# Performance work log

Hardware: AMD Instinct MI355X
Metric: run time of the kernel (lower is better)

## Reference

```python
import jax, jax.numpy as jnp
import numpy as np
from jax import lax

B, C, H, W = 16, 3, 512, 512


def _nms(heat):
    # 3x3 max-pool, stride 1, SAME padding; keep only local peaks
    hmax = lax.reduce_window(heat, -jnp.inf, lax.max,
                             (1, 1, 3, 3), (1, 1, 1, 1), 'SAME')
    return heat * (hmax == heat).astype(heat.dtype)


def _topk(scores, K):
    b, c, h, w = scores.shape
    # per-class topk over the spatial plane
    topk_scores, topk_inds = lax.top_k(scores.reshape(b, c, h * w), K)  # [b,c,K]
    topk_row = (topk_inds // w).astype(scores.dtype)
    topk_col = (topk_inds % w).astype(scores.dtype)
    # global topk across (class, K)
    topk_score, topk_ind = lax.top_k(topk_scores.reshape(b, c * K), K)  # [b,K]
    topk_clses = topk_ind // K
    gath = lambda x: jnp.take_along_axis(x.reshape(b, c * K), topk_ind, axis=1)
    return topk_score, gath(topk_inds), topk_clses, gath(topk_row), gath(topk_col)


def _transpose_and_gather_feat(feat, inds):
    b, ch, h, w = feat.shape
    f = feat.transpose(0, 2, 3, 1).reshape(b, h * w, ch)  # [b,HW,ch]
    return jnp.take_along_axis(f, inds[:, :, None], axis=1)  # [b,K,ch]


def _decode(hm, cen_offset, direction, z_coor, dim, K):
    b = hm.shape[0]
    hm = _nms(hm)
    scores, inds, clses, row, col = _topk(hm, K)
    off = _transpose_and_gather_feat(cen_offset, inds)           # [b,K,2]
    col = col[:, :, None] + off[:, :, 0:1]
    row = row[:, :, None] + off[:, :, 1:2]
    direction = _transpose_and_gather_feat(direction, inds)      # [b,K,2]
    z_coor = _transpose_and_gather_feat(z_coor, inds)            # [b,K,1]
    dim = _transpose_and_gather_feat(dim, inds)                  # [b,K,3]
    clses = clses[:, :, None].astype(hm.dtype)
    scores = scores[:, :, None]
    return jnp.concatenate([scores, col, row, z_coor, dim, direction, clses], axis=2)


def setup_inputs() -> dict:
    key = jax.random.key(0)
    k1, k2, k3, k4, k5 = jax.random.split(key, 5)
    return {
        'hm_cen': jax.random.normal(k1, (B, C, H, W), jnp.float32),
        'cen_offset': jax.random.normal(k2, (B, 2, H, W), jnp.float32),
        'direction': jax.random.normal(k3, (B, 2, H, W), jnp.float32),
        'z_coor': jax.random.normal(k4, (B, 1, H, W), jnp.float32),
        'dim': jax.random.normal(k5, (B, 3, H, W), jnp.float32),
        'K': 500,
    }


def reference(hm_cen, cen_offset, direction, z_coor, dim, K):
    # postprocessing_v2 applies sigmoid to the class heatmap before decode
    heat = jax.nn.sigmoid(hm_cen)
    return _decode(heat, cen_offset, direction, z_coor, dim, K)  # [B,K,10]
```

## Files before the change

kernel.cpp:

```cpp
#include <hip/hip_runtime.h>
#include <math.h>
#include <float.h>

#define Hd 512
#define Wd 512
#define HWp (Hd*Wd)
#define Bn 16
#define Cn 3
#define NMAP (Bn*Cn)
#define KTOP 500
#define P_SPLIT 8
#define BAND 64
#define SCAP 4096

__device__ __forceinline__ uint32_t flipbits(float v){
  uint32_t u = __float_as_uint(v);
  return u ^ (0x80000000u | (uint32_t)(-(int32_t)(u>>31)));
}
__device__ __forceinline__ float unflipbits(uint32_t f){
  uint32_t u = f ^ ((f>>31)? 0x80000000u : 0xFFFFFFFFu);
  return __uint_as_float(u);
}

__device__ __forceinline__ void nms_row(
    const float4 p0, const float4 p1, const float4 c0, const float4 c1,
    const float4 n0, const float4 n1, const int lane,
    uint32_t& pk, float* cv)
{
  float vm0 = fmaxf(fmaxf(p0.x,c0.x),n0.x);
  float vm1 = fmaxf(fmaxf(p0.y,c0.y),n0.y);
  float vm2 = fmaxf(fmaxf(p0.z,c0.z),n0.z);
  float vm3 = fmaxf(fmaxf(p0.w,c0.w),n0.w);
  float vm4 = fmaxf(fmaxf(p1.x,c1.x),n1.x);
  float vm5 = fmaxf(fmaxf(p1.y,c1.y),n1.y);
  float vm6 = fmaxf(fmaxf(p1.z,c1.z),n1.z);
  float vm7 = fmaxf(fmaxf(p1.w,c1.w),n1.w);
  float vmL = __shfl_up(vm7, 1);   if (lane == 0)  vmL = -INFINITY;
  float vmR = __shfl_down(vm0, 1); if (lane == 63) vmR = -INFINITY;

  float m0 = fmaxf(vmL, fmaxf(vm0, vm1));
  float m1 = fmaxf(vm0, fmaxf(vm1, vm2));
  float m2 = fmaxf(vm1, fmaxf(vm2, vm3));
  float m3 = fmaxf(vm2, fmaxf(vm3, vm4));
  float m4 = fmaxf(vm3, fmaxf(vm4, vm5));
  float m5 = fmaxf(vm4, fmaxf(vm5, vm6));
  float m6 = fmaxf(vm5, fmaxf(vm6, vm7));
  float m7 = fmaxf(vm6, fmaxf(vm7, vmR));

  pk = 0;
  if (c0.x >= m0) pk |= 1u;
  if (c0.y >= m1) pk |= 2u;
  if (c0.z >= m2) pk |= 4u;
  if (c0.w >= m3) pk |= 8u;
  if (c1.x >= m4) pk |= 16u;
  if (c1.y >= m5) pk |= 32u;
  if (c1.z >= m6) pk |= 64u;
  if (c1.w >= m7) pk |= 128u;
  cv[0]=c0.x; cv[1]=c0.y; cv[2]=c0.z; cv[3]=c0.w;
  cv[4]=c1.x; cv[5]=c1.y; cv[6]=c1.z; cv[7]=c1.w;
}

__device__ __forceinline__ void findT512(
    const uint32_t* hist, const uint32_t target, const int tid, const int lane,
    const int wid, uint32_t* wtot, uint32_t* res)
{
  const uint32_t s = hist[2*tid] + hist[2*tid+1];
  uint32_t v = s;
  #pragma unroll
  for (int d = 1; d < 64; d <<= 1) { uint32_t u = __shfl_down(v, d); if (lane + d < 64) v += u; }
  if (lane == 0) wtot[wid] = v;
  __syncthreads();
  uint32_t above = 0;
  for (int ww = wid + 1; ww < 8; ++ww) above += wtot[ww];
  const uint32_t gsuf = v + above;
  if (gsuf >= target && (gsuf - s) < target) {
    uint32_t cum = gsuf - s;
    for (int b = 2*tid + 1; b >= 2*tid; --b) {
      cum += hist[b];
      if (cum >= target) { res[0]=(uint32_t)b; res[1]=target-(cum-hist[b]); res[2]=cum; break; }
    }
  }
  __syncthreads();
}

__device__ __forceinline__ uint64_t cexch(uint64_t mine, uint64_t part, bool wantMax) {
  uint64_t mx = mine > part ? mine : part;
  uint64_t mn = mine > part ? part : mine;
  return wantMax ? mx : mn;
}

__device__ void bitonic512_reg(uint64_t& e0, uint64_t* sbuf, int tid, int lane)
{
  for (int k = 2; k <= 512; k <<= 1) {
    for (int j = k >> 1; j > 0; j >>= 1) {
      const bool up = ((tid & k) == 0);
      if (j >= 64) {
        __syncthreads();
        sbuf[tid] = e0;
        __syncthreads();
        uint64_t q = sbuf[tid ^ j];
        e0 = cexch(e0, q, up == ((tid & j) == 0));
      } else {
        uint64_t q = __shfl_xor((unsigned long long)e0, j);
        e0 = cexch(e0, q, up == ((lane & j) == 0));
      }
    }
  }
  __syncthreads();
  sbuf[tid] = e0;
  __syncthreads();
}

__device__ void sort1024_lds(uint64_t* a, int tid)
{
  for (int k = 2; k <= 1024; k <<= 1) {
    for (int j = k >> 1; j > 0; j >>= 1) {
      __syncthreads();
      const int lj = 31 - __clz(j);
      const int i  = ((tid >> lj) << (lj + 1)) | (tid & (j - 1));
      const int ixj = i | j;
      const uint64_t x = a[i], y = a[ixj];
      const bool up = ((i & k) == 0);
      const bool sw = up ? (x < y) : (x > y);
      if (sw) { a[i] = y; a[ixj] = x; }
    }
  }
  __syncthreads();
}

__global__ __launch_bounds__(512) void k_fused(
    const float* __restrict__ hm, uint64_t* __restrict__ l500)
{
  __shared__ uint64_t sbuf[SCAP];
  __shared__ uint32_t hist[1024];
  __shared__ uint32_t wtot[16];
  __shared__ uint32_t res[4];
  __shared__ uint32_t cnt1;

  const int m = blockIdx.x >> 3, p = blockIdx.x & (P_SPLIT - 1);
  const int tid = threadIdx.x, lane = tid & 63, w = tid >> 6;
  const float* map = hm + (size_t)m * HWp;
  const int xb = lane * 8;

  for (int i = tid; i < 1024; i += 512) hist[i] = 0;
  if (tid == 0) cnt1 = 0;
  __syncthreads();

  const float4 NEG4 = make_float4(-INFINITY,-INFINITY,-INFINITY,-INFINITY);
  #pragma unroll
  for (int sub = 0; sub < 2; ++sub) {
    const int y0 = p * BAND + w * 8 + sub * 4;
    float4 ra[6], rb[6];
    #pragma unroll
    for (int r = 0; r < 6; ++r) {
      const int yy = y0 - 1 + r;
      if (yy >= 0 && yy < Hd) {
        const float* rp = map + (size_t)yy * Wd + xb;
        ra[r] = *(const float4*)rp; rb[r] = *(const float4*)(rp + 4);
      } else { ra[r] = NEG4; rb[r] = NEG4; }
    }
    #pragma unroll
    for (int r = 0; r < 4; ++r) {
      uint32_t pk; float cv[8];
      nms_row(ra[r], rb[r], ra[r+1], rb[r+1], ra[r+2], rb[r+2], lane, pk, cv);
      const uint32_t np = (uint32_t)__popc(pk);
      uint32_t incl = np;
      #pragma unroll
      for (int d = 1; d < 64; d <<= 1) { uint32_t u = __shfl_up(incl, d); if (lane >= d) incl += u; }
      const uint32_t tot = __shfl(incl, 63);
      if (!tot) continue;
      uint32_t b0 = 0;
      if (lane == 0) b0 = atomicAdd(&cnt1, tot);
      b0 = __shfl(b0, 0);
      uint32_t pos = b0 + incl - np;
      const uint32_t ib = (uint32_t)((y0 + r) * Wd + xb);
      #pragma unroll
      for (int i = 0; i < 8; ++i) {
        if ((pk >> i) & 1u) {
          if (pos < (uint32_t)SCAP)
            sbuf[pos] = ((uint64_t)flipbits(cv[i]) << 32) | (uint32_t)(~(ib + (uint32_t)i));
          ++pos;
        }
      }
    }
  }
  __syncthreads();
  const uint32_t n = cnt1;
  const uint32_t nc = (n < (uint32_t)SCAP) ? n : (uint32_t)SCAP;

  uint32_t thresh20 = 0;
  if (n > 512) {
    for (uint32_t i = (uint32_t)tid; i < nc; i += 512u)
      atomicAdd(&hist[(uint32_t)(sbuf[i] >> 54)], 1u);
    __syncthreads();
    findT512(hist, KTOP, tid, lane, w, wtot, res);
    const uint32_t T1 = res[0], krem = res[1];
    for (int i = tid; i < 1024; i += 512) hist[i] = 0;
    __syncthreads();
    for (uint32_t i = (uint32_t)tid; i < nc; i += 512u) {
      const uint32_t f = (uint32_t)(sbuf[i] >> 32);
      if ((f >> 22) == T1) atomicAdd(&hist[(f >> 12) & 1023u], 1u);
    }
    __syncthreads();
    findT512(hist, krem, tid, lane, w, wtot, res);
    thresh20 = (T1 << 10) | res[0];
  }

  uint64_t sk0,sk1,sk2,sk3,sk4,sk5,sk6,sk7;
  bool kp0,kp1,kp2,kp3,kp4,kp5,kp6,kp7;
  {
    const uint32_t i0=(uint32_t)tid, i1=i0+512u, i2=i0+1024u, i3=i0+1536u,
                   i4=i0+2048u, i5=i0+2560u, i6=i0+3072u, i7=i0+3584u;
    sk0=sbuf[i0]; sk1=sbuf[i1]; sk2=sbuf[i2]; sk3=sbuf[i3];
    sk4=sbuf[i4]; sk5=sbuf[i5]; sk6=sbuf[i6]; sk7=sbuf[i7];
    kp0=(i0<nc)&&((uint32_t)(sk0>>44)>=thresh20);
    kp1=(i1<nc)&&((uint32_t)(sk1>>44)>=thresh20);
    kp2=(i2<nc)&&((uint32_t)(sk2>>44)>=thresh20);
    kp3=(i3<nc)&&((uint32_t)(sk3>>44)>=thresh20);
    kp4=(i4<nc)&&((uint32_t)(sk4>>44)>=thresh20);
    kp5=(i5<nc)&&((uint32_t)(sk5>>44)>=thresh20);
    kp6=(i6<nc)&&((uint32_t)(sk6>>44)>=thresh20);
    kp7=(i7<nc)&&((uint32_t)(sk7>>44)>=thresh20);
  }
  __syncthreads();

  const uint32_t c = (uint32_t)kp0+(uint32_t)kp1+(uint32_t)kp2+(uint32_t)kp3
                   + (uint32_t)kp4+(uint32_t)kp5+(uint32_t)kp6+(uint32_t)kp7;
  uint32_t incl = c;
  #pragma unroll
  for (int d = 1; d < 64; d <<= 1) { uint32_t u = __shfl_up(incl, d); if (lane >= d) incl += u; }
  if (lane == 63) wtot[w] = incl;
  __syncthreads();
  uint32_t base = incl - c, Mtot = 0;
  #pragma unroll
  for (int ww = 0; ww < 8; ++ww) { const uint32_t t = wtot[ww]; if (ww < w) base += t; Mtot += t; }
  {
    uint32_t o = base;
    if (kp0) { if (o < 1024u) sbuf[o] = sk0; ++o; }
    if (kp1) { if (o < 1024u) sbuf[o] = sk1; ++o; }
    if (kp2) { if (o < 1024u) sbuf[o] = sk2; ++o; }
    if (kp3) { if (o < 1024u) sbuf[o] = sk3; ++o; }
    if (kp4) { if (o < 1024u) sbuf[o] = sk4; ++o; }
    if (kp5) { if (o < 1024u) sbuf[o] = sk5; ++o; }
    if (kp6) { if (o < 1024u) sbuf[o] = sk6; ++o; }
    if (kp7) { if (o < 1024u) sbuf[o] = sk7; ++o; }
  }
  __syncthreads();
  uint32_t M = (Mtot < 1024u) ? Mtot : 1024u;

  if (M <= 512u) {
    uint64_t e0 = (tid < (int)M) ? sbuf[tid] : 0ull;
    bitonic512_reg(e0, sbuf, tid, lane);
  } else {
    for (int i = (int)M + tid; i < 1024; i += 512) sbuf[i] = 0ull;
    sort1024_lds(sbuf, tid);
  }

  l500[(size_t)blockIdx.x * 512 + tid] = sbuf[tid];
}

__global__ __launch_bounds__(1024) void k_merge(
    const uint64_t* __restrict__ l500,
    float* __restrict__ s1_scores, uint32_t* __restrict__ s1_inds)
{
  __shared__ uint64_t ld[P_SPLIT * 512];
  const int m = blockIdx.x >> 1, h = blockIdx.x & 1;
  const int tid = threadIdx.x;
  const uint64_t* src = l500 + (size_t)m * (P_SPLIT * 512);
  for (int i = tid; i < P_SPLIT * 512; i += 1024) ld[i] = src[i];
  __syncthreads();

  #pragma unroll
  for (int e = 0; e < 2; ++e) {
    const int i = h * 2048 + e * 1024 + tid;
    const uint64_t kk = ld[i];
    const int r = i & 511, L = i >> 9;
    if (kk != 0ull && r < KTOP) {
      uint32_t pos[P_SPLIT - 1];
      #pragma unroll
      for (int d = 0; d < P_SPLIT - 1; ++d) pos[d] = 0;
      #pragma unroll
      for (int s = 512; s >= 1; s >>= 1) {
        #pragma unroll
        for (int d = 0; d < P_SPLIT - 1; ++d) {
          const uint64_t* lst = ld + (((L + 1 + d) & (P_SPLIT - 1)) << 9);
          const uint32_t idx = pos[d] + (uint32_t)s - 1u;
          const uint64_t v = (idx < 512u) ? lst[idx] : 0ull;
          if (v > kk) pos[d] += (uint32_t)s;
        }
      }
      uint32_t rank = (uint32_t)r;
      #pragma unroll
      for (int d = 0; d < P_SPLIT - 1; ++d) rank += pos[d];
      if (rank < KTOP) {
        const float v = unflipbits((uint32_t)(kk >> 32));
        s1_scores[m * 512 + rank] = 1.0f / (1.0f + expf(-v));
        s1_inds [m * 512 + rank] = ~(uint32_t)kk;
      }
    }
  }
}

__global__ __launch_bounds__(512) void k_final(
    const float* __restrict__ s1_scores, const uint32_t* __restrict__ s1_inds,
    const float* __restrict__ cen_offset, const float* __restrict__ direction,
    const float* __restrict__ z_coor, const float* __restrict__ dimf,
    float* __restrict__ out)
{
  __shared__ float ssc[Cn][KTOP];
  const int b = blockIdx.x / Cn, c = blockIdx.x % Cn;
  const int tid = threadIdx.x;

  for (int i = tid; i < Cn * KTOP; i += 512) {
    int cc = i / KTOP, r = i - cc * KTOP;
    ssc[cc][r] = s1_scores[(b * Cn + cc) * 512 + r];
  }
  __syncthreads();

  if (tid < KTOP) {
    const int r = tid;
    const int i = c * KTOP + r;
    const uint64_t mykey = ((uint64_t)flipbits(ssc[c][r]) << 32) | (uint32_t)(~(uint32_t)i);
    int rank = r;
    #pragma unroll
    for (int cd = 1; cd < Cn; ++cd) {
      const int cc = (c + cd) % Cn;
      int lo = 0, hi = KTOP;
      while (lo < hi) {
        int mid = (lo + hi) >> 1;
        uint64_t k2 = ((uint64_t)flipbits(ssc[cc][mid]) << 32)
                    | (uint32_t)(~(uint32_t)(cc * KTOP + mid));
        if (k2 > mykey) lo = mid + 1; else hi = mid;
      }
      rank += lo;
    }
    if (rank < KTOP) {
      const float* co = cen_offset + (size_t)b * 2 * HWp;
      const float* di = direction  + (size_t)b * 2 * HWp;
      const float* zc = z_coor     + (size_t)b * HWp;
      const float* dm = dimf       + (size_t)b * 3 * HWp;
      const int bcx = b * Cn + c;
      const uint32_t ind = s1_inds[bcx * 512 + r];
      float o[10];
      o[0] = ssc[c][r];
      o[1] = (float)(ind & (Wd - 1)) + co[ind];
      o[2] = (float)(ind >> 9) + co[HWp + ind];
      o[3] = zc[ind];
      o[4] = dm[ind];
      o[5] = dm[HWp + ind];
      o[6] = dm[2 * HWp + ind];
      o[7] = di[ind];
      o[8] = di[HWp + ind];
      o[9] = (float)c;
      float* op = out + ((size_t)b * KTOP + rank) * 10;
      #pragma unroll
      for (int q = 0; q < 10; ++q) op[q] = o[q];
    }
  }
}

extern "C" void kernel_launch(void* const* d_in, const int* in_sizes, int n_in,
                              void* d_out, int out_size, void* d_ws, size_t ws_size,
                              hipStream_t stream)
{
  const float* hm         = (const float*)d_in[0];
  const float* cen_offset = (const float*)d_in[1];
  const float* direction  = (const float*)d_in[2];
  const float* z_coor     = (const float*)d_in[3];
  const float* dimf       = (const float*)d_in[4];
  float* out = (float*)d_out;

  char* ws = (char*)d_ws;
  uint64_t* l500  = (uint64_t*)ws;
  size_t o1       = (size_t)NMAP * P_SPLIT * 512 * 8;
  float*    s1_sc = (float*)(ws + o1);
  uint32_t* s1_id = (uint32_t*)(ws + o1 + (size_t)NMAP * 512 * 4);

  k_fused<<<NMAP * P_SPLIT, 512, 0, stream>>>(hm, l500);
  k_merge<<<NMAP * 2,       1024, 0, stream>>>(l500, s1_sc, s1_id);
  k_final<<<Bn * Cn,         512, 0, stream>>>(s1_sc, s1_id, cen_offset, direction, z_coor, dimf, out);
}
```

Baseline: 52.01 us.

## Replace bitonic sorts with rank-by-counting sort and ballot-based prefix sums

The wave-level prefix sums (shuffle scans) used for compaction are replaced by per-bit ballots plus masked popcounts, with readfirstlane for the broadcast. The bitonic sort of the surviving candidates (register/LDS 512-wide or LDS 1024-wide) is replaced by a rank sort: each thread counts how many candidates exceed its key and scatters the key to that rank. The intent is fewer barriers and shuffles. In exchange each thread does O(M) LDS broadcast reads, and the sort relies on keys being unique, which the packed index guarantees.

```diff
diff --git a/kernel.cpp b/kernel.cpp
--- a/kernel.cpp
+++ b/kernel.cpp
@@ -20,6 +20,9 @@
 __device__ __forceinline__ float unflipbits(uint32_t f){
   uint32_t u = f ^ ((f>>31)? 0x80000000u : 0xFFFFFFFFu);
   return __uint_as_float(u);
+}
+__device__ __forceinline__ uint32_t bcast0(uint32_t v){
+  return (uint32_t)__builtin_amdgcn_readfirstlane((int)v);
 }
 
 __device__ __forceinline__ void nms_row(
@@ -83,51 +86,6 @@
   __syncthreads();
 }
 
-__device__ __forceinline__ uint64_t cexch(uint64_t mine, uint64_t part, bool wantMax) {
-  uint64_t mx = mine > part ? mine : part;
-  uint64_t mn = mine > part ? part : mine;
-  return wantMax ? mx : mn;
-}
-
-__device__ void bitonic512_reg(uint64_t& e0, uint64_t* sbuf, int tid, int lane)
-{
-  for (int k = 2; k <= 512; k <<= 1) {
-    for (int j = k >> 1; j > 0; j >>= 1) {
-      const bool up = ((tid & k) == 0);
-      if (j >= 64) {
-        __syncthreads();
-        sbuf[tid] = e0;
-        __syncthreads();
-        uint64_t q = sbuf[tid ^ j];
-        e0 = cexch(e0, q, up == ((tid & j) == 0));
-      } else {
-        uint64_t q = __shfl_xor((unsigned long long)e0, j);
-        e0 = cexch(e0, q, up == ((lane & j) == 0));
-      }
-    }
-  }
-  __syncthreads();
-  sbuf[tid] = e0;
-  __syncthreads();
-}
-
-__device__ void sort1024_lds(uint64_t* a, int tid)
-{
-  for (int k = 2; k <= 1024; k <<= 1) {
-    for (int j = k >> 1; j > 0; j >>= 1) {
-      __syncthreads();
-      const int lj = 31 - __clz(j);
-      const int i  = ((tid >> lj) << (lj + 1)) | (tid & (j - 1));
-      const int ixj = i | j;
-      const uint64_t x = a[i], y = a[ixj];
-      const bool up = ((i & k) == 0);
-      const bool sw = up ? (x < y) : (x > y);
-      if (sw) { a[i] = y; a[ixj] = x; }
-    }
-  }
-  __syncthreads();
-}
-
 __global__ __launch_bounds__(512) void k_fused(
     const float* __restrict__ hm, uint64_t* __restrict__ l500)
 {
@@ -139,6 +97,7 @@
 
   const int m = blockIdx.x >> 3, p = blockIdx.x & (P_SPLIT - 1);
   const int tid = threadIdx.x, lane = tid & 63, w = tid >> 6;
+  const uint64_t lt = (1ull << lane) - 1ull;
   const float* map = hm + (size_t)m * HWp;
   const int xb = lane * 8;
 
@@ -164,15 +123,17 @@
       uint32_t pk; float cv[8];
       nms_row(ra[r], rb[r], ra[r+1], rb[r+1], ra[r+2], rb[r+2], lane, pk, cv);
       const uint32_t np = (uint32_t)__popc(pk);
-      uint32_t incl = np;
-      #pragma unroll
-      for (int d = 1; d < 64; d <<= 1) { uint32_t u = __shfl_up(incl, d); if (lane >= d) incl += u; }
-      const uint32_t tot = __shfl(incl, 63);
+      const uint64_t B0 = __ballot((np & 1u) != 0u);
+      const uint64_t B1 = __ballot((np & 2u) != 0u);
+      const uint64_t B2 = __ballot((np & 4u) != 0u);
+      const uint32_t tot = (uint32_t)__popcll(B0) + 2u*(uint32_t)__popcll(B1)
+                         + 4u*(uint32_t)__popcll(B2);
       if (!tot) continue;
       uint32_t b0 = 0;
       if (lane == 0) b0 = atomicAdd(&cnt1, tot);
-      b0 = __shfl(b0, 0);
-      uint32_t pos = b0 + incl - np;
+      b0 = bcast0(b0);
+      uint32_t pos = b0 + (uint32_t)__popcll(B0 & lt) + 2u*(uint32_t)__popcll(B1 & lt)
+                        + 4u*(uint32_t)__popcll(B2 & lt);
       const uint32_t ib = (uint32_t)((y0 + r) * Wd + xb);
       #pragma unroll
       for (int i = 0; i < 8; ++i) {
@@ -226,12 +187,17 @@
 
   const uint32_t c = (uint32_t)kp0+(uint32_t)kp1+(uint32_t)kp2+(uint32_t)kp3
                    + (uint32_t)kp4+(uint32_t)kp5+(uint32_t)kp6+(uint32_t)kp7;
-  uint32_t incl = c;
-  #pragma unroll
-  for (int d = 1; d < 64; d <<= 1) { uint32_t u = __shfl_up(incl, d); if (lane >= d) incl += u; }
-  if (lane == 63) wtot[w] = incl;
-  __syncthreads();
-  uint32_t base = incl - c, Mtot = 0;
+  const uint64_t C0 = __ballot((c & 1u) != 0u);
+  const uint64_t C1 = __ballot((c & 2u) != 0u);
+  const uint64_t C2 = __ballot((c & 4u) != 0u);
+  const uint64_t C3 = __ballot((c & 8u) != 0u);
+  const uint32_t wsum = (uint32_t)__popcll(C0) + 2u*(uint32_t)__popcll(C1)
+                      + 4u*(uint32_t)__popcll(C2) + 8u*(uint32_t)__popcll(C3);
+  const uint32_t excl = (uint32_t)__popcll(C0 & lt) + 2u*(uint32_t)__popcll(C1 & lt)
+                      + 4u*(uint32_t)__popcll(C2 & lt) + 8u*(uint32_t)__popcll(C3 & lt);
+  if (lane == 0) wtot[w] = wsum;
+  __syncthreads();
+  uint32_t base = excl, Mtot = 0;
   #pragma unroll
   for (int ww = 0; ww < 8; ++ww) { const uint32_t t = wtot[ww]; if (ww < w) base += t; Mtot += t; }
   {
@@ -246,17 +212,29 @@
     if (kp7) { if (o < 1024u) sbuf[o] = sk7; ++o; }
   }
   __syncthreads();
-  uint32_t M = (Mtot < 1024u) ? Mtot : 1024u;
-
-  if (M <= 512u) {
-    uint64_t e0 = (tid < (int)M) ? sbuf[tid] : 0ull;
-    bitonic512_reg(e0, sbuf, tid, lane);
-  } else {
-    for (int i = (int)M + tid; i < 1024; i += 512) sbuf[i] = 0ull;
-    sort1024_lds(sbuf, tid);
-  }
-
-  l500[(size_t)blockIdx.x * 512 + tid] = sbuf[tid];
+  const uint32_t M  = (Mtot < 1024u) ? Mtot : 1024u;
+  const uint32_t Mp = (M + 3u) & ~3u;
+
+  if ((uint32_t)tid < Mp - M) sbuf[M + (uint32_t)tid] = 0ull;
+  sbuf[2048 + tid] = 0ull;
+  __syncthreads();
+
+  const uint64_t mine0 = ((uint32_t)tid < M) ? sbuf[tid] : 0ull;
+  const uint64_t mine1 = ((uint32_t)tid + 512u < M) ? sbuf[tid + 512u] : 0ull;
+  uint32_t r0 = 0, r1 = 0;
+  for (uint32_t j = 0; j < Mp; j += 4u) {
+    const uint64_t a = sbuf[j], b = sbuf[j+1], cj = sbuf[j+2], d = sbuf[j+3];
+    r0 += (a > mine0) ? 1u : 0u; r0 += (b > mine0) ? 1u : 0u;
+    r0 += (cj > mine0) ? 1u : 0u; r0 += (d > mine0) ? 1u : 0u;
+    r1 += (a > mine1) ? 1u : 0u; r1 += (b > mine1) ? 1u : 0u;
+    r1 += (cj > mine1) ? 1u : 0u; r1 += (d > mine1) ? 1u : 0u;
+  }
+  __syncthreads();
+  if ((uint32_t)tid < M && r0 < 512u) sbuf[2048 + r0] = mine0;
+  if ((uint32_t)tid + 512u < M && r1 < 512u) sbuf[2048 + r1] = mine1;
+  __syncthreads();
+
+  l500[(size_t)blockIdx.x * 512 + tid] = sbuf[2048 + tid];
 }
 
 __global__ __launch_bounds__(1024) void k_merge(
```

Measured after the change: 58.43 us. +12.3%, slower.
